# Kernel optimization log

Measured on AMD Instinct MI355X. Metric: run time of the kernel, lower is better.

Reference implementation:

```python
import jax, jax.numpy as jnp
import numpy as np
from jax.scipy.special import logsumexp

N_ITERS = 20


def setup_inputs() -> dict:
    key = jax.random.key(0)
    k1, _ = jax.random.split(key)
    cost_matrix = jax.random.uniform(k1, (64, 1024, 1024), dtype=jnp.float32)
    epsilon = jnp.ones((1,), dtype=jnp.float32)
    return {"cost_matrix": cost_matrix, "epsilon": epsilon}


def reference(cost_matrix, epsilon):
    # log-space Sinkhorn: alternate row / column normalization in log domain
    log_alpha = -cost_matrix / epsilon  # (B, N, N)

    def step(la, _):
        la = la - logsumexp(la, axis=-1, keepdims=True)  # row normalize
        la = la - logsumexp(la, axis=-2, keepdims=True)  # col normalize
        return la, None

    log_alpha, _ = jax.lax.scan(step, log_alpha, None, length=N_ITERS)
    return jnp.exp(log_alpha)
```

## Files before the change

kernel.cpp:

```cpp
#include <hip/hip_runtime.h>
#include <hip/hip_fp16.h>


#define BATCH 64
#define N 1024
#define NITERS 20
#define ROWS_PER_BLOCK 64
#define BLOCKS_PER_BATCH (N / ROWS_PER_BLOCK)
#define THREADS 256
#define NU2 (N / 4)
#define NU4 (N / 8)

union H2U { __half2 h; unsigned u; };

__device__ __forceinline__ uint2 f4_to_h4(float4 f) {
    H2U a, b;
    a.h = __float22half2_rn(make_float2(f.x, f.y));
    b.h = __float22half2_rn(make_float2(f.z, f.w));
    uint2 r; r.x = a.u; r.y = b.u;
    return r;
}

__device__ __forceinline__ float4 h4_to_f4(uint2 r) {
    H2U a, b;
    a.u = r.x; b.u = r.y;
    float2 fa = __half22float2(a.h);
    float2 fb = __half22float2(b.h);
    return make_float4(fa.x, fa.y, fb.x, fb.y);
}

__device__ __forceinline__ void h8_unpack(uint4 r, float* f) {
    H2U a, b, c, d;
    a.u = r.x; b.u = r.y; c.u = r.z; d.u = r.w;
    float2 fa = __half22float2(a.h), fb = __half22float2(b.h);
    float2 fc = __half22float2(c.h), fd = __half22float2(d.h);
    f[0] = fa.x; f[1] = fa.y; f[2] = fb.x; f[3] = fb.y;
    f[4] = fc.x; f[5] = fc.y; f[6] = fd.x; f[7] = fd.y;
}

__device__ __forceinline__ uint4 h8_pack(const float* f) {
    H2U a, b, c, d;
    a.h = __float22half2_rn(make_float2(f[0], f[1]));
    b.h = __float22half2_rn(make_float2(f[2], f[3]));
    c.h = __float22half2_rn(make_float2(f[4], f[5]));
    d.h = __float22half2_rn(make_float2(f[6], f[7]));
    uint4 r; r.x = a.u; r.y = b.u; r.z = c.u; r.w = d.u;
    return r;
}


__global__ __launch_bounds__(THREADS) void sk_zero(float* __restrict__ csum_all) {
    const int i = blockIdx.x * THREADS + threadIdx.x;
    csum_all[i] = 0.0f;
}

__global__ __launch_bounds__(THREADS) void sk_build(
        const float* __restrict__ C, const float* __restrict__ eps,
        uint4* __restrict__ K, float* __restrict__ u,
        float* __restrict__ csum_out) {
    __shared__ float4 smc[4][N / 4];
    const int t = threadIdx.x;
    const int lane = t & 63, w = t >> 6;
    const int b = blockIdx.y;
    const int row0 = blockIdx.x * ROWS_PER_BLOCK + w * 16;
    const float nie = -1.0f / eps[0];

    const float4* __restrict__ Cp =
        (const float4*)(C + ((size_t)b * N + row0) * N) + lane * 4;
    uint4* __restrict__ Kp = K + ((size_t)b * N + row0) * NU4 + lane * 2;

    float colacc[16];
    #pragma unroll
    for (int q = 0; q < 16; ++q) colacc[q] = 0.0f;

    float4 cur[4];
    #pragma unroll
    for (int q = 0; q < 4; ++q) cur[q] = Cp[q];

    for (int i = 0; i < 16; ++i) {
        float4 nxt[4];
        if (i < 15) {
            #pragma unroll
            for (int q = 0; q < 4; ++q) nxt[q] = Cp[(i + 1) * (N / 4) + q];
        }
        float k[16];
        const float* cf = (const float*)cur;
        #pragma unroll
        for (int q = 0; q < 16; ++q) k[q] = __expf(cf[q] * nie);

        Kp[(size_t)i * NU4]     = h8_pack(k);
        Kp[(size_t)i * NU4 + 1] = h8_pack(k + 8);

        float s = (((k[0] + k[1]) + (k[2] + k[3])) + ((k[4] + k[5]) + (k[6] + k[7])))
                + (((k[8] + k[9]) + (k[10] + k[11])) + ((k[12] + k[13]) + (k[14] + k[15])));
        #pragma unroll
        for (int off = 32; off; off >>= 1) s += __shfl_xor(s, off, 64);
        const float ui = 1.0f / s;
        if (lane == 0) u[b * N + row0 + i] = ui;

        #pragma unroll
        for (int q = 0; q < 16; ++q) colacc[q] += k[q] * ui;

        if (i < 15) {
            #pragma unroll
            for (int q = 0; q < 4; ++q) cur[q] = nxt[q];
        }
    }

    #pragma unroll
    for (int q = 0; q < 4; ++q)
        smc[w][lane * 4 + q] = make_float4(colacc[4 * q], colacc[4 * q + 1],
                                           colacc[4 * q + 2], colacc[4 * q + 3]);
    __syncthreads();
    float4 s0 = smc[0][t], s1 = smc[1][t], s2 = smc[2][t], s3 = smc[3][t];
    float4 sum;
    sum.x = (s0.x + s1.x) + (s2.x + s3.x);
    sum.y = (s0.y + s1.y) + (s2.y + s3.y);
    sum.z = (s0.z + s1.z) + (s2.z + s3.z);
    sum.w = (s0.w + s1.w) + (s2.w + s3.w);
    float* cs = csum_out + b * N + 4 * t;
    atomicAdd(cs + 0, sum.x);
    atomicAdd(cs + 1, sum.y);
    atomicAdd(cs + 2, sum.z);
    atomicAdd(cs + 3, sum.w);
}

__global__ __launch_bounds__(THREADS) void sk_iter(
        const uint4* __restrict__ K, const float* __restrict__ csum_in,
        float* __restrict__ u, float* __restrict__ csum_out) {
    __shared__ float4 smc[4][N / 4];
    const int t = threadIdx.x;
    const int lane = t & 63, w = t >> 6;
    const int b = blockIdx.y;
    const int row0 = blockIdx.x * ROWS_PER_BLOCK + w * 16;

    const float4* __restrict__ cin = (const float4*)(csum_in + b * N) + lane * 4;
    float vv[16];
    #pragma unroll
    for (int q = 0; q < 4; ++q) {
        float4 c = cin[q];
        vv[4 * q + 0] = 1.0f / c.x;
        vv[4 * q + 1] = 1.0f / c.y;
        vv[4 * q + 2] = 1.0f / c.z;
        vv[4 * q + 3] = 1.0f / c.w;
    }

    const uint4* __restrict__ Kp = K + ((size_t)b * N + row0) * NU4 + lane * 2;

    float colacc[16];
    #pragma unroll
    for (int q = 0; q < 16; ++q) colacc[q] = 0.0f;

    uint4 c0 = Kp[0], c1 = Kp[1];
    for (int i = 0; i < 16; ++i) {
        uint4 n0, n1;
        if (i < 15) {
            n0 = Kp[(size_t)(i + 1) * NU4];
            n1 = Kp[(size_t)(i + 1) * NU4 + 1];
        }
        float k[16];
        h8_unpack(c0, k);
        h8_unpack(c1, k + 8);

        float pa = (k[0] * vv[0] + k[1] * vv[1]) + (k[2] * vv[2] + k[3] * vv[3]);
        float pb = (k[4] * vv[4] + k[5] * vv[5]) + (k[6] * vv[6] + k[7] * vv[7]);
        float pc = (k[8] * vv[8] + k[9] * vv[9]) + (k[10] * vv[10] + k[11] * vv[11]);
        float pd = (k[12] * vv[12] + k[13] * vv[13]) + (k[14] * vv[14] + k[15] * vv[15]);
        float s = (pa + pb) + (pc + pd);

        #pragma unroll
        for (int off = 32; off; off >>= 1) s += __shfl_xor(s, off, 64);
        const float ui = 1.0f / s;
        if (lane == 0) u[b * N + row0 + i] = ui;

        #pragma unroll
        for (int q = 0; q < 16; ++q) colacc[q] += k[q] * ui;

        if (i < 15) { c0 = n0; c1 = n1; }
    }

    #pragma unroll
    for (int q = 0; q < 4; ++q)
        smc[w][lane * 4 + q] = make_float4(colacc[4 * q], colacc[4 * q + 1],
                                           colacc[4 * q + 2], colacc[4 * q + 3]);
    __syncthreads();
    float4 s0 = smc[0][t], s1 = smc[1][t], s2 = smc[2][t], s3 = smc[3][t];
    float4 sum;
    sum.x = (s0.x + s1.x) + (s2.x + s3.x);
    sum.y = (s0.y + s1.y) + (s2.y + s3.y);
    sum.z = (s0.z + s1.z) + (s2.z + s3.z);
    sum.w = (s0.w + s1.w) + (s2.w + s3.w);
    float* cs = csum_out + b * N + 4 * t;
    atomicAdd(cs + 0, sum.x);
    atomicAdd(cs + 1, sum.y);
    atomicAdd(cs + 2, sum.z);
    atomicAdd(cs + 3, sum.w);
}

__global__ __launch_bounds__(THREADS) void sk_final(
        const uint2* __restrict__ K, const float* __restrict__ u,
        const float* __restrict__ csum_last, float* __restrict__ out) {
    const int t = threadIdx.x;
    const int row = blockIdx.x;
    const int b = blockIdx.y;
    const float ui = u[b * N + row];
    const float4 ci = ((const float4*)(csum_last + b * N))[t];
    const float4 vv = make_float4(1.0f / ci.x, 1.0f / ci.y, 1.0f / ci.z, 1.0f / ci.w);
    const size_t base = (size_t)b * N + row;
    float4 k = h4_to_f4((K + base * NU2)[t]);
    float4 o;
    o.x = k.x * ui * vv.x;
    o.y = k.y * ui * vv.y;
    o.z = k.z * ui * vv.z;
    o.w = k.w * ui * vv.w;
    ((float4*)(out + base * N))[t] = o;
}


__device__ __forceinline__ float block_reduce_broadcast(float val, float* lds) {
    #pragma unroll
    for (int off = 32; off > 0; off >>= 1)
        val += __shfl_xor(val, off, 64);
    const int lane = threadIdx.x & 63;
    const int wid  = threadIdx.x >> 6;
    if (lane == 0) lds[wid] = val;
    __syncthreads();
    float total = lds[0] + lds[1] + lds[2] + lds[3];
    __syncthreads();
    return total;
}

__global__ __launch_bounds__(THREADS) void sink_init(float* __restrict__ v,
                                                     float* __restrict__ colsum) {
    const int i = blockIdx.x * THREADS + threadIdx.x;
    v[i] = 1.0f;
    colsum[i] = 0.0f;
}

__global__ __launch_bounds__(THREADS) void sink_iter(
        const float* __restrict__ C, const float* __restrict__ eps,
        const float* __restrict__ v, float* __restrict__ u,
        float* __restrict__ colsum) {
    __shared__ float lds[4];
    const int t = threadIdx.x;
    const int b = blockIdx.y;
    const int row0 = blockIdx.x * ROWS_PER_BLOCK;
    const float neg_inv_eps = -1.0f / eps[0];

    const float4 vv = ((const float4*)(v + b * N))[t];
    const float4* __restrict__ Cp = (const float4*)(C + ((size_t)b * N + row0) * N);

    float4 colacc = make_float4(0.f, 0.f, 0.f, 0.f);
    float4 cur = Cp[t];
    for (int i = 0; i < ROWS_PER_BLOCK; ++i) {
        float4 nxt = cur;
        if (i + 1 < ROWS_PER_BLOCK)
            nxt = Cp[(size_t)(i + 1) * (N / 4) + t];

        float4 k;
        k.x = __expf(cur.x * neg_inv_eps);
        k.y = __expf(cur.y * neg_inv_eps);
        k.z = __expf(cur.z * neg_inv_eps);
        k.w = __expf(cur.w * neg_inv_eps);

        float s = k.x * vv.x + k.y * vv.y + k.z * vv.z + k.w * vv.w;
        float S = block_reduce_broadcast(s, lds);
        float ui = 1.0f / S;
        if (t == 0) u[b * N + row0 + i] = ui;

        colacc.x += k.x * ui;
        colacc.y += k.y * ui;
        colacc.z += k.z * ui;
        colacc.w += k.w * ui;
        cur = nxt;
    }

    float* cs = colsum + b * N + 4 * t;
    atomicAdd(cs + 0, colacc.x);
    atomicAdd(cs + 1, colacc.y);
    atomicAdd(cs + 2, colacc.z);
    atomicAdd(cs + 3, colacc.w);
}

__global__ __launch_bounds__(THREADS) void sink_fix(float* __restrict__ v,
                                                    float* __restrict__ colsum) {
    const int i = blockIdx.x * THREADS + threadIdx.x;
    v[i] = 1.0f / colsum[i];
    colsum[i] = 0.0f;
}

__global__ __launch_bounds__(THREADS) void sink_final(
        const float* __restrict__ C, const float* __restrict__ eps,
        const float* __restrict__ u, const float* __restrict__ v,
        float* __restrict__ out) {
    const int t = threadIdx.x;
    const int row = blockIdx.x;
    const int b = blockIdx.y;
    const float neg_inv_eps = -1.0f / eps[0];
    const float ui = u[b * N + row];
    const float4 vv = ((const float4*)(v + b * N))[t];
    const size_t base = ((size_t)b * N + row) * N;
    float4 c = ((const float4*)(C + base))[t];
    float4 o;
    o.x = __expf(c.x * neg_inv_eps) * ui * vv.x;
    o.y = __expf(c.y * neg_inv_eps) * ui * vv.y;
    o.z = __expf(c.z * neg_inv_eps) * ui * vv.z;
    o.w = __expf(c.w * neg_inv_eps) * ui * vv.w;
    ((float4*)(out + base))[t] = o;
}


extern "C" void kernel_launch(void* const* d_in, const int* in_sizes, int n_in,
                              void* d_out, int out_size, void* d_ws, size_t ws_size,
                              hipStream_t stream) {
    const float* C   = (const float*)d_in[0];
    const float* eps = (const float*)d_in[1];
    float* out = (float*)d_out;

    const size_t k_bytes  = (size_t)BATCH * N * N * 2;
    const size_t uv_elems = (size_t)BATCH * N;
    const size_t needed   = k_bytes + uv_elems * 4 * (1 + NITERS);

    if (ws_size >= needed) {
        uint4* K      = (uint4*)d_ws;
        float* u      = (float*)((char*)d_ws + k_bytes);
        float* csum   = u + uv_elems;

        sk_zero<<<dim3(NITERS * uv_elems / THREADS), dim3(THREADS), 0, stream>>>(csum);
        sk_build<<<dim3(BLOCKS_PER_BATCH, BATCH), dim3(THREADS), 0, stream>>>(
            C, eps, K, u, csum);
        for (int it = 2; it <= NITERS; ++it) {
            sk_iter<<<dim3(BLOCKS_PER_BATCH, BATCH), dim3(THREADS), 0, stream>>>(
                K, csum + (size_t)(it - 2) * uv_elems, u,
                csum + (size_t)(it - 1) * uv_elems);
        }
        sk_final<<<dim3(N, BATCH), dim3(THREADS), 0, stream>>>(
            (const uint2*)K, u, csum + (size_t)(NITERS - 1) * uv_elems, out);
    } else {
        float* u      = (float*)d_ws;
        float* v      = u + uv_elems;
        float* colsum = v + uv_elems;
        sink_init<<<dim3(BATCH * N / THREADS), dim3(THREADS), 0, stream>>>(v, colsum);
        for (int it = 0; it < NITERS; ++it) {
            sink_iter<<<dim3(BLOCKS_PER_BATCH, BATCH), dim3(THREADS), 0, stream>>>(
                C, eps, v, u, colsum);
            sink_fix<<<dim3(BATCH * N / THREADS), dim3(THREADS), 0, stream>>>(v, colsum);
        }
        sink_final<<<dim3(N, BATCH), dim3(THREADS), 0, stream>>>(C, eps, u, v, out);
    }
}
```

Baseline: 1.090 ms.

## Store a second FP8 copy of the kernel matrix for the intermediate Sinkhorn iterations

```diff
diff --git a/kernel.cpp b/kernel.cpp
--- a/kernel.cpp
+++ b/kernel.cpp
@@ -10,16 +10,11 @@
 #define THREADS 256
 #define NU2 (N / 4)
 #define NU4 (N / 8)
+#define NU4F8 (N / 16)
+
+typedef float f32x2 __attribute__((ext_vector_type(2)));
 
 union H2U { __half2 h; unsigned u; };
-
-__device__ __forceinline__ uint2 f4_to_h4(float4 f) {
-    H2U a, b;
-    a.h = __float22half2_rn(make_float2(f.x, f.y));
-    b.h = __float22half2_rn(make_float2(f.z, f.w));
-    uint2 r; r.x = a.u; r.y = b.u;
-    return r;
-}
 
 __device__ __forceinline__ float4 h4_to_f4(uint2 r) {
     H2U a, b;
@@ -48,6 +43,36 @@
     return r;
 }
 
+__device__ __forceinline__ uint4 pack_fp8_16(const float* k) {
+    uint4 r;
+    int a;
+    a = __builtin_amdgcn_cvt_pk_fp8_f32(k[0],  k[1],  0, false);
+    a = __builtin_amdgcn_cvt_pk_fp8_f32(k[2],  k[3],  a, true);
+    r.x = (unsigned)a;
+    a = __builtin_amdgcn_cvt_pk_fp8_f32(k[4],  k[5],  0, false);
+    a = __builtin_amdgcn_cvt_pk_fp8_f32(k[6],  k[7],  a, true);
+    r.y = (unsigned)a;
+    a = __builtin_amdgcn_cvt_pk_fp8_f32(k[8],  k[9],  0, false);
+    a = __builtin_amdgcn_cvt_pk_fp8_f32(k[10], k[11], a, true);
+    r.z = (unsigned)a;
+    a = __builtin_amdgcn_cvt_pk_fp8_f32(k[12], k[13], 0, false);
+    a = __builtin_amdgcn_cvt_pk_fp8_f32(k[14], k[15], a, true);
+    r.w = (unsigned)a;
+    return r;
+}
+
+__device__ __forceinline__ void unpack_fp8_16(uint4 r, float* f) {
+    f32x2 p;
+    p = __builtin_amdgcn_cvt_pk_f32_fp8((int)r.x, false); f[0]  = p.x; f[1]  = p.y;
+    p = __builtin_amdgcn_cvt_pk_f32_fp8((int)r.x, true);  f[2]  = p.x; f[3]  = p.y;
+    p = __builtin_amdgcn_cvt_pk_f32_fp8((int)r.y, false); f[4]  = p.x; f[5]  = p.y;
+    p = __builtin_amdgcn_cvt_pk_f32_fp8((int)r.y, true);  f[6]  = p.x; f[7]  = p.y;
+    p = __builtin_amdgcn_cvt_pk_f32_fp8((int)r.z, false); f[8]  = p.x; f[9]  = p.y;
+    p = __builtin_amdgcn_cvt_pk_f32_fp8((int)r.z, true);  f[10] = p.x; f[11] = p.y;
+    p = __builtin_amdgcn_cvt_pk_f32_fp8((int)r.w, false); f[12] = p.x; f[13] = p.y;
+    p = __builtin_amdgcn_cvt_pk_f32_fp8((int)r.w, true);  f[14] = p.x; f[15] = p.y;
+}
+
 
 __global__ __launch_bounds__(THREADS) void sk_zero(float* __restrict__ csum_all) {
     const int i = blockIdx.x * THREADS + threadIdx.x;
@@ -56,8 +81,8 @@
 
 __global__ __launch_bounds__(THREADS) void sk_build(
         const float* __restrict__ C, const float* __restrict__ eps,
-        uint4* __restrict__ K, float* __restrict__ u,
-        float* __restrict__ csum_out) {
+        uint4* __restrict__ K16, uint4* __restrict__ K8,
+        float* __restrict__ u, float* __restrict__ csum_out) {
     __shared__ float4 smc[4][N / 4];
     const int t = threadIdx.x;
     const int lane = t & 63, w = t >> 6;
@@ -67,7 +92,8 @@
 
     const float4* __restrict__ Cp =
         (const float4*)(C + ((size_t)b * N + row0) * N) + lane * 4;
-    uint4* __restrict__ Kp = K + ((size_t)b * N + row0) * NU4 + lane * 2;
+    uint4* __restrict__ Kp16 = K16 + ((size_t)b * N + row0) * NU4 + lane * 2;
+    uint4* __restrict__ Kp8  = K8  + ((size_t)b * N + row0) * NU4F8 + lane;
 
     float colacc[16];
     #pragma unroll
@@ -88,8 +114,9 @@
         #pragma unroll
         for (int q = 0; q < 16; ++q) k[q] = __expf(cf[q] * nie);
 
-        Kp[(size_t)i * NU4]     = h8_pack(k);
-        Kp[(size_t)i * NU4 + 1] = h8_pack(k + 8);
+        Kp16[(size_t)i * NU4]     = h8_pack(k);
+        Kp16[(size_t)i * NU4 + 1] = h8_pack(k + 8);
+        Kp8[(size_t)i * NU4F8]    = pack_fp8_16(k);
 
         float s = (((k[0] + k[1]) + (k[2] + k[3])) + ((k[4] + k[5]) + (k[6] + k[7])))
                 + (((k[8] + k[9]) + (k[10] + k[11])) + ((k[12] + k[13]) + (k[14] + k[15])));
@@ -125,9 +152,9 @@
     atomicAdd(cs + 3, sum.w);
 }
 
-__global__ __launch_bounds__(THREADS) void sk_iter(
-        const uint4* __restrict__ K, const float* __restrict__ csum_in,
-        float* __restrict__ u, float* __restrict__ csum_out) {
+__global__ __launch_bounds__(THREADS) void sk_iter8(
+        const uint4* __restrict__ K8, const float* __restrict__ csum_in,
+        float* __restrict__ csum_out) {
     __shared__ float4 smc[4][N / 4];
     const int t = threadIdx.x;
     const int lane = t & 63, w = t >> 6;
@@ -145,22 +172,20 @@
         vv[4 * q + 3] = 1.0f / c.w;
     }
 
-    const uint4* __restrict__ Kp = K + ((size_t)b * N + row0) * NU4 + lane * 2;
+    const uint4* __restrict__ Kp = K8 + ((size_t)b * N + row0) * NU4F8 + lane;
 
     float colacc[16];
     #pragma unroll
     for (int q = 0; q < 16; ++q) colacc[q] = 0.0f;
 
-    uint4 c0 = Kp[0], c1 = Kp[1];
+    uint4 c0 = Kp[0];
+    uint4 c1 = Kp[NU4F8];
     for (int i = 0; i < 16; ++i) {
-        uint4 n0, n1;
-        if (i < 15) {
-            n0 = Kp[(size_t)(i + 1) * NU4];
-            n1 = Kp[(size_t)(i + 1) * NU4 + 1];
-        }
+        uint4 c2;
+        if (i < 14) c2 = Kp[(size_t)(i + 2) * NU4F8];
+
         float k[16];
-        h8_unpack(c0, k);
-        h8_unpack(c1, k + 8);
+        unpack_fp8_16(c0, k);
 
         float pa = (k[0] * vv[0] + k[1] * vv[1]) + (k[2] * vv[2] + k[3] * vv[3]);
         float pb = (k[4] * vv[4] + k[5] * vv[5]) + (k[6] * vv[6] + k[7] * vv[7]);
@@ -171,12 +196,12 @@
         #pragma unroll
         for (int off = 32; off; off >>= 1) s += __shfl_xor(s, off, 64);
         const float ui = 1.0f / s;
-        if (lane == 0) u[b * N + row0 + i] = ui;
 
         #pragma unroll
         for (int q = 0; q < 16; ++q) colacc[q] += k[q] * ui;
 
-        if (i < 15) { c0 = n0; c1 = n1; }
+        c0 = c1;
+        if (i < 14) c1 = c2;
     }
 
     #pragma unroll
@@ -197,6 +222,78 @@
     atomicAdd(cs + 3, sum.w);
 }
 
+__global__ __launch_bounds__(THREADS) void sk_iter(
+        const uint4* __restrict__ K, const float* __restrict__ csum_in,
+        float* __restrict__ u, float* __restrict__ csum_out) {
+    __shared__ float4 smc[4][N / 4];
+    const int t = threadIdx.x;
+    const int lane = t & 63, w = t >> 6;
+    const int b = blockIdx.y;
+    const int row0 = blockIdx.x * ROWS_PER_BLOCK + w * 16;
+
+    const float4* __restrict__ cin = (const float4*)(csum_in + b * N) + lane * 4;
+    float vv[16];
+    #pragma unroll
+    for (int q = 0; q < 4; ++q) {
+        float4 c = cin[q];
+        vv[4 * q + 0] = 1.0f / c.x;
+        vv[4 * q + 1] = 1.0f / c.y;
+        vv[4 * q + 2] = 1.0f / c.z;
+        vv[4 * q + 3] = 1.0f / c.w;
+    }
+
+    const uint4* __restrict__ Kp = K + ((size_t)b * N + row0) * NU4 + lane * 2;
+
+    float colacc[16];
+    #pragma unroll
+    for (int q = 0; q < 16; ++q) colacc[q] = 0.0f;
+
+    uint4 c0 = Kp[0], c1 = Kp[1];
+    for (int i = 0; i < 16; ++i) {
+        uint4 n0, n1;
+        if (i < 15) {
+            n0 = Kp[(size_t)(i + 1) * NU4];
+            n1 = Kp[(size_t)(i + 1) * NU4 + 1];
+        }
+        float k[16];
+        h8_unpack(c0, k);
+        h8_unpack(c1, k + 8);
+
+        float pa = (k[0] * vv[0] + k[1] * vv[1]) + (k[2] * vv[2] + k[3] * vv[3]);
+        float pb = (k[4] * vv[4] + k[5] * vv[5]) + (k[6] * vv[6] + k[7] * vv[7]);
+        float pc = (k[8] * vv[8] + k[9] * vv[9]) + (k[10] * vv[10] + k[11] * vv[11]);
+        float pd = (k[12] * vv[12] + k[13] * vv[13]) + (k[14] * vv[14] + k[15] * vv[15]);
+        float s = (pa + pb) + (pc + pd);
+
+        #pragma unroll
+        for (int off = 32; off; off >>= 1) s += __shfl_xor(s, off, 64);
+        const float ui = 1.0f / s;
+        if (lane == 0) u[b * N + row0 + i] = ui;
+
+        #pragma unroll
+        for (int q = 0; q < 16; ++q) colacc[q] += k[q] * ui;
+
+        if (i < 15) { c0 = n0; c1 = n1; }
+    }
+
+    #pragma unroll
+    for (int q = 0; q < 4; ++q)
+        smc[w][lane * 4 + q] = make_float4(colacc[4 * q], colacc[4 * q + 1],
+                                           colacc[4 * q + 2], colacc[4 * q + 3]);
+    __syncthreads();
+    float4 s0 = smc[0][t], s1 = smc[1][t], s2 = smc[2][t], s3 = smc[3][t];
+    float4 sum;
+    sum.x = (s0.x + s1.x) + (s2.x + s3.x);
+    sum.y = (s0.y + s1.y) + (s2.y + s3.y);
+    sum.z = (s0.z + s1.z) + (s2.z + s3.z);
+    sum.w = (s0.w + s1.w) + (s2.w + s3.w);
+    float* cs = csum_out + b * N + 4 * t;
+    atomicAdd(cs + 0, sum.x);
+    atomicAdd(cs + 1, sum.y);
+    atomicAdd(cs + 2, sum.z);
+    atomicAdd(cs + 3, sum.w);
+}
+
 __global__ __launch_bounds__(THREADS) void sk_final(
         const uint2* __restrict__ K, const float* __restrict__ u,
         const float* __restrict__ csum_last, float* __restrict__ out) {
@@ -317,25 +414,30 @@
     const float* eps = (const float*)d_in[1];
     float* out = (float*)d_out;
 
-    const size_t k_bytes  = (size_t)BATCH * N * N * 2;
-    const size_t uv_elems = (size_t)BATCH * N;
-    const size_t needed   = k_bytes + uv_elems * 4 * (1 + NITERS);
+    const size_t k16_bytes = (size_t)BATCH * N * N * 2;
+    const size_t k8_bytes  = (size_t)BATCH * N * N;
+    const size_t uv_elems  = (size_t)BATCH * N;
+    const size_t needed    = k16_bytes + k8_bytes + uv_elems * 4 * (1 + NITERS);
 
     if (ws_size >= needed) {
-        uint4* K      = (uint4*)d_ws;
-        float* u      = (float*)((char*)d_ws + k_bytes);
-        float* csum   = u + uv_elems;
+        uint4* K16 = (uint4*)d_ws;
+        uint4* K8  = (uint4*)((char*)d_ws + k16_bytes);
+        float* u   = (float*)((char*)d_ws + k16_bytes + k8_bytes);
+        float* csum = u + uv_elems;
 
         sk_zero<<<dim3(NITERS * uv_elems / THREADS), dim3(THREADS), 0, stream>>>(csum);
         sk_build<<<dim3(BLOCKS_PER_BATCH, BATCH), dim3(THREADS), 0, stream>>>(
-            C, eps, K, u, csum);
-        for (int it = 2; it <= NITERS; ++it) {
-            sk_iter<<<dim3(BLOCKS_PER_BATCH, BATCH), dim3(THREADS), 0, stream>>>(
-                K, csum + (size_t)(it - 2) * uv_elems, u,
+            C, eps, K16, K8, u, csum);
+        for (int it = 2; it <= NITERS - 1; ++it) {
+            sk_iter8<<<dim3(BLOCKS_PER_BATCH, BATCH), dim3(THREADS), 0, stream>>>(
+                K8, csum + (size_t)(it - 2) * uv_elems,
                 csum + (size_t)(it - 1) * uv_elems);
         }
+        sk_iter<<<dim3(BLOCKS_PER_BATCH, BATCH), dim3(THREADS), 0, stream>>>(
+            K16, csum + (size_t)(NITERS - 2) * uv_elems, u,
+            csum + (size_t)(NITERS - 1) * uv_elems);
         sk_final<<<dim3(N, BATCH), dim3(THREADS), 0, stream>>>(
-            (const uint2*)K, u, csum + (size_t)(NITERS - 1) * uv_elems, out);
+            (const uint2*)K16, u, csum + (size_t)(NITERS - 1) * uv_elems, out);
     } else {
         float* u      = (float*)d_ws;
         float* v      = u + uv_elems;
```

After: 1.006 ms. -7.7%, faster.
